# Kernel optimization log

Measured on AMD Instinct MI355X. Metric: run time of the kernel, lower is better.

The kernel has to match this reference:

```python
import jax, jax.numpy as jnp
import numpy as np

# db1 (Haar) filters, replicating the torch module's pywt-derived constants.
_s = np.float32(1.0 / np.sqrt(2.0))
_dl = np.array([_s, _s], np.float32)    # dec_lo[::-1]
_dh = np.array([_s, -_s], np.float32)   # dec_hi[::-1]
_rl = np.array([_s, _s], np.float32)    # rec_lo
_rh = np.array([_s, -_s], np.float32)   # rec_hi
# filters[k][i,j] = a[j]*b[i]  (torch: a.unsqueeze(0)*b.unsqueeze(1)) == outer(b, a)
DEC = jnp.asarray(np.stack([np.outer(_dl, _dl) / 2.0, np.outer(_dh, _dl), np.outer(_dl, _dh), np.outer(_dh, _dh)], 0))  # [4,2,2]
REC = jnp.asarray(np.stack([np.outer(_rl, _rl) * 2.0, np.outer(_rh, _rl), np.outer(_rl, _rh), np.outer(_rh, _rh)], 0))  # [4,2,2]


def wt(x):
    # stride-2 2x2 conv per channel == linear mix of 2x2 blocks; fused over all channels
    B, C, H, W = x.shape
    xb = x.reshape(B, C, H // 2, 2, W // 2, 2)
    y = jnp.einsum('kpq,bchpwq->bckhw', DEC, xb)  # [B,C,4,H/2,W/2]
    y = jnp.concatenate([y[:, :, :1], (y[:, :, 1:] + 1.0) * 0.5], axis=2)  # rescale HF bands
    return y.reshape(B, 4 * C, H // 2, W // 2)


def iwt(y):
    B, C4, H, W = y.shape
    C = C4 // 4
    yb = y.reshape(B, C, 4, H, W)
    yb = jnp.concatenate([yb[:, :, :1], 2.0 * yb[:, :, 1:] - 1.0], axis=2)  # undo HF rescale
    x = jnp.einsum('kpq,bckhw->bchpwq', REC, yb)  # conv_transpose2d, stride 2, no overlap
    return x.reshape(B, C, 2 * H, 2 * W)


def conv3x3(x, w, b):
    y = jax.lax.conv_general_dilated(x, w, (1, 1), ((1, 1), (1, 1)), dimension_numbers=('NCHW', 'OIHW', 'NCHW'))
    return y + b[None, :, None, None]


def setup_inputs() -> dict:
    key = jax.random.key(0)
    ks = jax.random.split(key, 20)
    B, Cin, H, W = 8, 1, 512, 512
    c = 16
    inp = {'x': jax.random.normal(ks[0], (B, Cin, H, W), jnp.float32)}
    specs = [('conv1', c, 4 * Cin), ('conv2', 4 * c, 4 * c), ('conv3', 16 * c, 16 * c), ('conv4', 64 * c, 64 * c),
             ('convd1', 4, c), ('convd2', c, 2 * c), ('convd3', 4 * c, 8 * c), ('convd4', 16 * c, 32 * c)]
    for idx, (name, o, i) in enumerate(specs):
        kw, kb = jax.random.split(ks[1 + idx])
        inp[name + '_w'] = jax.random.normal(kw, (o, i, 3, 3), jnp.float32) / np.float32(np.sqrt(i * 9))
        inp[name + '_b'] = jax.random.normal(kb, (o,), jnp.float32) * 0.01
    return inp


def reference(x, conv1_w, conv1_b, conv2_w, conv2_b, conv3_w, conv3_b, conv4_w, conv4_b,
              convd1_w, convd1_b, convd2_w, convd2_b, convd3_w, convd3_b, convd4_w, convd4_b):
    lrelu = lambda t: jax.nn.leaky_relu(t, 0.2)
    w1 = wt(x);  c1 = lrelu(conv3x3(w1, conv1_w, conv1_b))
    w2 = wt(c1); c2 = lrelu(conv3x3(w2, conv2_w, conv2_b))
    w3 = wt(c2); c3 = lrelu(conv3x3(w3, conv3_w, conv3_b))
    w4 = wt(c3); c4 = lrelu(conv3x3(w4, conv4_w, conv4_b))
    c5 = lrelu(conv3x3(c4, conv4_w, conv4_b))  # conv4 reused, as in the torch module
    c6 = conv3x3(c5, conv4_w, conv4_b)
    ic4 = lrelu(c6 + w4)
    ic3 = lrelu(conv3x3(jnp.concatenate([c3, iwt(ic4)], 1), convd4_w, convd4_b))
    ic2 = lrelu(conv3x3(jnp.concatenate([c2, iwt(ic3)], 1), convd3_w, convd3_b))
    ic1 = lrelu(conv3x3(jnp.concatenate([c1, iwt(ic2)], 1), convd2_w, convd2_b))
    iw1 = lrelu(conv3x3(ic1, convd1_w, convd1_b))
    logits = iwt(iw1)
    return jax.nn.sigmoid(logits)
```

## Files before the change

kernel.cpp:

```cpp
#include <hip/hip_runtime.h>
#include <cstddef>


typedef unsigned short u16;
typedef unsigned int u32;
typedef __bf16 bf16x8 __attribute__((ext_vector_type(8)));
typedef float floatx4 __attribute__((ext_vector_type(4)));
typedef u16 u16x4 __attribute__((ext_vector_type(4)));
typedef u16 u16x8 __attribute__((ext_vector_type(8)));

__device__ __forceinline__ float b2f(u16 h) {
    union { u32 u; float f; } x; x.u = ((u32)h) << 16; return x.f;
}
__device__ __forceinline__ u16 f2b(float f) {
    union { float f; u32 u; } x; x.f = f;
    return (u16)((x.u + 0x7FFFu + ((x.u >> 16) & 1u)) >> 16);
}
__device__ __forceinline__ float lrelu_f(float v) { return v > 0.f ? v : 0.2f * v; }

__device__ __forceinline__ void gld16(const u16* g, u16* l) {
    __builtin_amdgcn_global_load_lds(
        (const __attribute__((address_space(1))) u32*)(const void*)g,
        (__attribute__((address_space(3))) u32*)(void*)l, 16, 0, 0);
}

__global__ __launch_bounds__(512, 4)
void conv_mfma8_k(const u16* __restrict__ in, int Cin, int iWp, int iImg,
                  const u16* __restrict__ wb, const float* __restrict__ bias,
                  const u16* __restrict__ skip, int sC, int sWp, int sImg, int spad,
                  u16* __restrict__ out, int Cst, int oWp, int oImg, int opad,
                  int logW, int logH)
{
    __shared__ alignas(16) u16 S[32768];

    const int tid = threadIdx.x;
    const int wid = tid >> 6, lane = tid & 63;
    const int half = wid >> 2, wl = wid & 3;
    const int W = 1 << logW, H = 1 << logH;
    const int mBase = blockIdx.x * 128;
    const int nBase = blockIdx.y * 128;
    const int K = 9 * Cin;
    const int nChunks = K / 32;
    const int nC = nChunks >> 1;

    const int kg = lane & 3;
    const int rr = lane >> 2;
    const int kgs = kg ^ ((rr >> 1) & 3);

    const int k0 = half * nC * 32;
    int tap = k0 / Cin;
    int cbn = k0 - tap * Cin;

    const u16 *gA0, *gA1, *gB0, *gB1;
    {
        int ty = tap / 3, tx = tap - ty * 3;
        int m0 = mBase + wl * 32 + rr;
        int px0 = m0 & (W - 1), py0 = (m0 >> logW) & (H - 1), pb0 = m0 >> (logW + logH);
        gA0 = in + ((size_t)pb0 * iImg + (size_t)(py0 + ty) * iWp + (px0 + tx)) * Cin + cbn + kgs * 8;
        int m1 = m0 + 16;
        int px1 = m1 & (W - 1), py1 = (m1 >> logW) & (H - 1), pb1 = m1 >> (logW + logH);
        gA1 = in + ((size_t)pb1 * iImg + (size_t)(py1 + ty) * iWp + (px1 + tx)) * Cin + cbn + kgs * 8;
    }
    gB0 = wb + (size_t)(nBase + wl * 32 + rr) * K + k0 + kgs * 8;
    gB1 = wb + (size_t)(nBase + wl * 32 + 16 + rr) * K + k0 + kgs * 8;

    u16* Sb = &S[half * 16384];
    u16* lA0 = Sb + wl * 1024;
    u16* lA1 = Sb + wl * 1024 + 512;
    u16* lB0 = Sb + 8192 + wl * 1024;
    u16* lB1 = Sb + 8192 + wl * 1024 + 512;

    const int wm = wl >> 1, wn = wl & 1;
    const int fm = lane & 15;
    const int fk = ((lane >> 4) * 8) ^ (((fm >> 1) & 3) << 3);

    floatx4 acc[4][4] = {};

    const size_t rowStep = (size_t)(iWp - 2) * Cin;

    auto stage = [&](int buf) {
        gld16(gA0, lA0 + buf * 4096);
        gld16(gA1, lA1 + buf * 4096);
        gld16(gB0, lB0 + buf * 4096);
        gld16(gB1, lB1 + buf * 4096);
        size_t dA = 32;
        cbn += 32;
        if (cbn == Cin) { cbn = 0; ++tap; dA = ((tap % 3 == 0) ? rowStep : (size_t)Cin) - (size_t)(Cin - 32); }
        gA0 += dA; gA1 += dA;
        gB0 += 32; gB1 += 32;
    };

    auto compute = [&](int buf) {
        const u16* Ab = Sb + buf * 4096;
        const u16* Bb = Sb + 8192 + buf * 4096;
        bf16x8 af[4], bfr[4];
#pragma unroll
        for (int mt = 0; mt < 4; ++mt)
            af[mt] = *(const bf16x8*)&Ab[(wm * 64 + mt * 16 + fm) * 32 + fk];
#pragma unroll
        for (int nt = 0; nt < 4; ++nt)
            bfr[nt] = *(const bf16x8*)&Bb[(wn * 64 + nt * 16 + fm) * 32 + fk];
        __builtin_amdgcn_s_setprio(1);
#pragma unroll
        for (int mt = 0; mt < 4; ++mt)
#pragma unroll
            for (int nt = 0; nt < 4; ++nt)
                acc[mt][nt] = __builtin_amdgcn_mfma_f32_16x16x32_bf16(af[mt], bfr[nt], acc[mt][nt], 0, 0, 0);
        __builtin_amdgcn_s_setprio(0);
    };

    stage(0);
    __syncthreads();
    for (int kc = 0; kc < nC; kc += 2) {
        stage(1);
        compute(0);
        __syncthreads();
        if (kc + 2 < nC) stage(0);
        compute(1);
        __syncthreads();
    }

    float* R = (float*)S;
    if (half == 1) {
#pragma unroll
        for (int mt = 0; mt < 4; ++mt)
#pragma unroll
            for (int nt = 0; nt < 4; ++nt) {
                int j = mt * 4 + nt;
                *(floatx4*)&R[(size_t)(((wl * 16 + j) * 64) + lane) * 4] = acc[mt][nt];
            }
    }
    __syncthreads();
    if (half == 0) {
        const int rq = (lane >> 4) * 4;
#pragma unroll
        for (int mt = 0; mt < 4; ++mt)
#pragma unroll
            for (int nt = 0; nt < 4; ++nt) {
                int j = mt * 4 + nt;
                floatx4 v = *(const floatx4*)&R[(size_t)(((wl * 16 + j) * 64) + lane) * 4];
                acc[mt][nt] = acc[mt][nt] + v;
            }
#pragma unroll
        for (int mt = 0; mt < 4; ++mt) {
            const int mrow = mBase + wm * 64 + mt * 16 + rq;
#pragma unroll
            for (int r = 0; r < 4; ++r) {
                int m2 = mrow + r;
                int px = m2 & (W - 1), py = (m2 >> logW) & (H - 1), pb2 = m2 >> (logW + logH);
                size_t ob = ((size_t)pb2 * oImg + (size_t)(py + opad) * oWp + (px + opad)) * Cst;
                size_t sb = 0;
                if (skip) sb = ((size_t)pb2 * sImg + (size_t)(py + spad) * sWp + (px + spad)) * sC;
#pragma unroll
                for (int nt = 0; nt < 4; ++nt) {
                    int n = nBase + wn * 64 + nt * 16 + fm;
                    float v = acc[mt][nt][r] + bias[n];
                    if (skip) v += b2f(skip[sb + n]);
                    v = lrelu_f(v);
                    out[ob + n] = f2b(v);
                }
            }
        }
    }
}

__global__ __launch_bounds__(256)
void conv_mfma_k(const u16* __restrict__ in, int Cin, int iWp, int iImg,
                 const u16* __restrict__ wb, const float* __restrict__ bias,
                 const u16* __restrict__ skip, int sC, int sWp, int sImg, int spad,
                 u16* __restrict__ out, int Cst, int oWp, int oImg, int opad,
                 int logW, int logH)
{
    constexpr int NT = 2;
    constexpr int BM = 128, BN = NT * 32;
    constexpr int ASZ = BM * 32;
    constexpr int BSZ = BN * 32;
    __shared__ u16 At[2 * ASZ];
    __shared__ u16 Bt[2 * BSZ];

    const int tid = threadIdx.x;
    const int wid = tid >> 6, lane = tid & 63;
    const int W = 1 << logW, H = 1 << logH;
    const int mBase = blockIdx.x * BM;
    const int nBase = blockIdx.y * BN;
    const int K = 9 * Cin;
    const int kg = lane & 3;
    const int rr = lane >> 2;
    const int kgs = kg ^ ((rr >> 1) & 3);

    const u16 *gA0, *gA1, *gB0;
    {
        int m0 = mBase + wid * 32 + rr;
        int px0 = m0 & (W - 1), py0 = (m0 >> logW) & (H - 1), pb0 = m0 >> (logW + logH);
        gA0 = in + ((size_t)pb0 * iImg + (size_t)py0 * iWp + px0) * Cin + kgs * 8;
        int m1 = m0 + 16;
        int px1 = m1 & (W - 1), py1 = (m1 >> logW) & (H - 1), pb1 = m1 >> (logW + logH);
        gA1 = in + ((size_t)pb1 * iImg + (size_t)py1 * iWp + px1) * Cin + kgs * 8;
    }
    gB0 = wb + (size_t)(nBase + wid * 16 + rr) * K + kgs * 8;
    u16* lA0 = &At[wid * 1024];
    u16* lA1 = &At[wid * 1024 + 512];
    u16* lB0 = &Bt[wid * 512];

    const int wm = wid >> 1, wn = wid & 1;
    const int fm = lane & 15;
    const int fk = ((lane >> 4) * 8) ^ (((fm >> 1) & 3) << 3);

    floatx4 acc[4][NT] = {};

    const int nChunks = K / 32;
    const size_t rowStep = (size_t)(iWp - 2) * Cin;
    int cbn = 0, tap = 0;

    auto stage = [&](int buf) {
        gld16(gA0, lA0 + buf * ASZ);
        gld16(gA1, lA1 + buf * ASZ);
        gld16(gB0, lB0 + buf * BSZ);
        size_t dA = 32;
        cbn += 32;
        if (cbn == Cin) { cbn = 0; ++tap; dA = ((tap % 3 == 0) ? rowStep : (size_t)Cin) - (size_t)(Cin - 32); }
        gA0 += dA; gA1 += dA;
        gB0 += 32;
    };

    auto compute = [&](int buf) {
        const u16* Ab = &At[buf * ASZ];
        const u16* Bb = &Bt[buf * BSZ];
        bf16x8 af[4], bfr[NT];
#pragma unroll
        for (int mt = 0; mt < 4; ++mt)
            af[mt] = *(const bf16x8*)&Ab[(wm * 64 + mt * 16 + fm) * 32 + fk];
#pragma unroll
        for (int nt = 0; nt < NT; ++nt)
            bfr[nt] = *(const bf16x8*)&Bb[(wn * (NT * 16) + nt * 16 + fm) * 32 + fk];
        __builtin_amdgcn_s_setprio(1);
#pragma unroll
        for (int mt = 0; mt < 4; ++mt)
#pragma unroll
            for (int nt = 0; nt < NT; ++nt)
                acc[mt][nt] = __builtin_amdgcn_mfma_f32_16x16x32_bf16(af[mt], bfr[nt], acc[mt][nt], 0, 0, 0);
        __builtin_amdgcn_s_setprio(0);
    };

    stage(0);
    __syncthreads();
    for (int kc = 0; kc < nChunks; kc += 2) {
        stage(1);
        compute(0);
        __syncthreads();
        if (kc + 2 < nChunks) stage(0);
        compute(1);
        __syncthreads();
    }

    const int rq = (lane >> 4) * 4;
#pragma unroll
    for (int mt = 0; mt < 4; ++mt) {
        const int mrow = mBase + wm * 64 + mt * 16 + rq;
#pragma unroll
        for (int r = 0; r < 4; ++r) {
            int m2 = mrow + r;
            int px = m2 & (W - 1), py = (m2 >> logW) & (H - 1), pb2 = m2 >> (logW + logH);
            size_t ob = ((size_t)pb2 * oImg + (size_t)(py + opad) * oWp + (px + opad)) * Cst;
            size_t sb = 0;
            if (skip) sb = ((size_t)pb2 * sImg + (size_t)(py + spad) * sWp + (px + spad)) * sC;
#pragma unroll
            for (int nt = 0; nt < NT; ++nt) {
                int n = nBase + wn * (NT * 16) + nt * 16 + fm;
                float v = acc[mt][nt][r] + bias[n];
                if (skip) v += b2f(skip[sb + n]);
                v = lrelu_f(v);
                out[ob + n] = f2b(v);
            }
        }
    }
}

__global__ __launch_bounds__(256)
void conv_n16_k(const u16* __restrict__ in, int iWp, int iImg,
                const u16* __restrict__ wb, const float* __restrict__ bias,
                u16* __restrict__ out, int logW, int logH)
{
    __shared__ u16 At[128 * 32];
    __shared__ u16 Bt[16 * 32];
    const int tid = threadIdx.x;
    const int wid = tid >> 6, lane = tid & 63;
    const int W = 1 << logW, H = 1 << logH;
    const int mBase = blockIdx.x * 128;
    const int kg = lane & 3, rr = lane >> 2;
    const int kgs = kg ^ ((rr >> 1) & 3);

    const u16 *gA0, *gA1;
    {
        int m0 = mBase + wid * 32 + rr;
        int px0 = m0 & (W - 1), py0 = (m0 >> logW) & (H - 1), pb0 = m0 >> (logW + logH);
        gA0 = in + ((size_t)pb0 * iImg + (size_t)py0 * iWp + px0) * 32 + kgs * 8;
        int m1 = m0 + 16;
        int px1 = m1 & (W - 1), py1 = (m1 >> logW) & (H - 1), pb1 = m1 >> (logW + logH);
        gA1 = in + ((size_t)pb1 * iImg + (size_t)py1 * iWp + px1) * 32 + kgs * 8;
    }
    const u16* gB = wb + (size_t)rr * 288 + kgs * 8;
    u16* lA0 = &At[wid * 1024];
    u16* lA1 = &At[wid * 1024 + 512];

    const int fm = lane & 15;
    const int fk = ((lane >> 4) * 8) ^ (((fm >> 1) & 3) << 3);
    floatx4 acc[2] = {};
    const size_t rowStep = (size_t)(iWp - 2) * 32;

    for (int tap = 0; tap < 9; ++tap) {
        gld16(gA0, lA0);
        gld16(gA1, lA1);
        if (wid == 0) gld16(gB, &Bt[0]);
        __syncthreads();
        bf16x8 bf = *(const bf16x8*)&Bt[fm * 32 + fk];
#pragma unroll
        for (int mt = 0; mt < 2; ++mt) {
            bf16x8 af = *(const bf16x8*)&At[(wid * 32 + mt * 16 + fm) * 32 + fk];
            acc[mt] = __builtin_amdgcn_mfma_f32_16x16x32_bf16(af, bf, acc[mt], 0, 0, 0);
        }
        __syncthreads();
        size_t dA = (tap % 3 == 2) ? rowStep : (size_t)32;
        gA0 += dA; gA1 += dA; gB += 32;
    }

    const int rq = (lane >> 4) * 4;
    const float bn = bias[fm];
#pragma unroll
    for (int mt = 0; mt < 2; ++mt) {
#pragma unroll
        for (int r = 0; r < 4; ++r) {
            int m2 = mBase + wid * 32 + mt * 16 + rq + r;
            out[(size_t)m2 * 16 + fm] = f2b(lrelu_f(acc[mt][r] + bn));
        }
    }
}

template<int CIN, int COUT>
__global__ __launch_bounds__(256)
void conv_direct_k(const u16* __restrict__ in, int Sin,
                   const float* __restrict__ w, const float* __restrict__ bias,
                   u16* __restrict__ out, int Sout, int oWp, int oImg, int opad,
                   int logW, int logH, int total)
{
    int m = blockIdx.x * 256 + threadIdx.x;
    if (m >= total) return;
    const int W = 1 << logW, H = 1 << logH;
    const int px = m & (W - 1);
    const int py = (m >> logW) & (H - 1);
    const int pb = m >> (logW + logH);
    float acc[COUT];
#pragma unroll
    for (int o = 0; o < COUT; ++o) acc[o] = bias[o];
    for (int tap = 0; tap < 9; ++tap) {
        int dy = tap / 3 - 1, dx = tap % 3 - 1;
        int iy = py + dy, ix = px + dx;
        if ((unsigned)iy >= (unsigned)H || (unsigned)ix >= (unsigned)W) continue;
        const u16* p = in + (size_t)((((pb << logH) + iy) << logW) + ix) * Sin;
        if constexpr (CIN == 4) {
            u16x4 v = *(const u16x4*)p;
#pragma unroll
            for (int ci = 0; ci < 4; ++ci) {
                float f = b2f(v[ci]);
#pragma unroll
                for (int o = 0; o < COUT; ++o) acc[o] += f * w[(o * CIN + ci) * 9 + tap];
            }
        } else {
#pragma unroll
            for (int c8 = 0; c8 < CIN / 8; ++c8) {
                u16x8 v = *(const u16x8*)(p + c8 * 8);
#pragma unroll
                for (int j = 0; j < 8; ++j) {
                    int ci = c8 * 8 + j;
                    float f = b2f(v[j]);
#pragma unroll
                    for (int o = 0; o < COUT; ++o) acc[o] += f * w[(o * CIN + ci) * 9 + tap];
                }
            }
        }
    }
    size_t ob = ((size_t)pb * oImg + (size_t)(py + opad) * oWp + (px + opad)) * Sout;
#pragma unroll
    for (int o = 0; o < COUT; ++o)
        out[ob + o] = f2b(lrelu_f(acc[o]));
}

__global__ __launch_bounds__(256)
void wt_in_k(const float* __restrict__ x, u16* __restrict__ out, int total)
{
    int idx = blockIdx.x * 256 + threadIdx.x;
    if (idx >= total) return;
    int wq = idx & 255, t = idx >> 8;
    int hq = t & 255, b = t >> 8;
    const float* p = x + ((size_t)b * 512 + 2 * hq) * 512 + 2 * wq;
    float a = p[0], bv = p[1], cv = p[512], d = p[513];
    u16x4 o = { f2b(0.25f * (a + bv + cv + d)),
                f2b(0.25f * (a + bv - cv - d) + 0.5f),
                f2b(0.25f * (a - bv + cv - d) + 0.5f),
                f2b(0.25f * (a - bv - cv + d) + 0.5f) };
    *(u16x4*)&out[(size_t)idx * 4] = o;
}

__global__ __launch_bounds__(256)
void wt_k(const u16* __restrict__ in, int Sin, int iWp, int iImg, int ipad,
          u16* __restrict__ out, int Sout, int oWp, int oImg, int opad,
          int logC, int logWo, int logHo, int total)
{
    int idx = blockIdx.x * 256 + threadIdx.x;
    if (idx >= total) return;
    const int C = 1 << logC, Wo = 1 << logWo, Ho = 1 << logHo;
    int c = idx & (C - 1); int t = idx >> logC;
    int wq = t & (Wo - 1); t >>= logWo;
    int hq = t & (Ho - 1); int b = t >> logHo;
    size_t p00 = ((size_t)b * iImg + (size_t)(2 * hq + ipad) * iWp + (2 * wq + ipad)) * Sin + c;
    float a  = b2f(in[p00]);
    float bv = b2f(in[p00 + Sin]);
    float cv = b2f(in[p00 + (size_t)iWp * Sin]);
    float d  = b2f(in[p00 + (size_t)iWp * Sin + Sin]);
    u16x4 o = { f2b(0.25f * (a + bv + cv + d)),
                f2b(0.25f * (a + bv - cv - d) + 0.5f),
                f2b(0.25f * (a - bv + cv - d) + 0.5f),
                f2b(0.25f * (a - bv - cv + d) + 0.5f) };
    *(u16x4*)&out[((size_t)b * oImg + (size_t)(hq + opad) * oWp + (wq + opad)) * Sout + 4 * c] = o;
}

__global__ __launch_bounds__(256)
void iwt_k(const u16* __restrict__ in, int Sin, int logC, int logW, int logH,
           u16* __restrict__ out, int Sout, int oWp, int oImg, int opad, int total)
{
    int idx = blockIdx.x * 256 + threadIdx.x;
    if (idx >= total) return;
    const int C = 1 << logC, W = 1 << logW;
    int c = idx & (C - 1); int t = idx >> logC;
    int wq = t & (W - 1); t >>= logW;
    int hq = t & ((1 << logH) - 1); int b = t >> logH;
    u16x4 v = *(const u16x4*)&in[(size_t)((((b << logH) + hq) << logW) + wq) * Sin + 4 * c];
    float y0 = b2f(v[0]);
    float y1 = 2.f * b2f(v[1]) - 1.f;
    float y2 = 2.f * b2f(v[2]) - 1.f;
    float y3 = 2.f * b2f(v[3]) - 1.f;
    float x00 = y0 + 0.5f * ( y1 + y2 + y3);
    float x01 = y0 + 0.5f * ( y1 - y2 - y3);
    float x10 = y0 + 0.5f * (-y1 + y2 - y3);
    float x11 = y0 + 0.5f * (-y1 - y2 + y3);
    size_t q = ((size_t)b * oImg + (size_t)(2 * hq + opad) * oWp + (2 * wq + opad)) * Sout + c;
    out[q] = f2b(x00);
    out[q + Sout] = f2b(x01);
    out[q + (size_t)oWp * Sout] = f2b(x10);
    out[q + (size_t)oWp * Sout + Sout] = f2b(x11);
}

__global__ __launch_bounds__(256)
void iwt_out_k(const u16* __restrict__ in, float* __restrict__ out, int total)
{
    int idx = blockIdx.x * 256 + threadIdx.x;
    if (idx >= total) return;
    int wq = idx & 255, t = idx >> 8;
    int hq = t & 255, b = t >> 8;
    u16x4 v = *(const u16x4*)&in[(size_t)idx * 4];
    float y0 = b2f(v[0]);
    float y1 = 2.f * b2f(v[1]) - 1.f;
    float y2 = 2.f * b2f(v[2]) - 1.f;
    float y3 = 2.f * b2f(v[3]) - 1.f;
    float x00 = y0 + 0.5f * ( y1 + y2 + y3);
    float x01 = y0 + 0.5f * ( y1 - y2 - y3);
    float x10 = y0 + 0.5f * (-y1 + y2 - y3);
    float x11 = y0 + 0.5f * (-y1 - y2 + y3);
    float* q = out + ((size_t)b * 512 + 2 * hq) * 512 + 2 * wq;
    q[0]   = 1.f / (1.f + __expf(-x00));
    q[1]   = 1.f / (1.f + __expf(-x01));
    q[512] = 1.f / (1.f + __expf(-x10));
    q[513] = 1.f / (1.f + __expf(-x11));
}

__global__ __launch_bounds__(256)
void prep_w_k(const float* __restrict__ src, u16* __restrict__ dst, int logCIN, int total)
{
    int idx = blockIdx.x * 256 + threadIdx.x;
    if (idx >= total) return;
    const int CIN = 1 << logCIN;
    int ci = idx & (CIN - 1);
    int q = idx >> logCIN;
    int tap = q % 9, o = q / 9;
    dst[idx] = f2b(src[((size_t)(o * CIN + ci)) * 9 + tap]);
}

__global__ __launch_bounds__(256)
void zb_k(u16* __restrict__ buf, int Wp, int Hp, int C, int total)
{
    int idx = blockIdx.x * 256 + threadIdx.x;
    if (idx >= total) return;
    int c8 = idx % (C / 8); int t = idx / (C / 8);
    int nbp = 2 * Wp + 2 * (Hp - 2);
    int p = t % nbp; int b = t / nbp;
    int y, x;
    if (p < Wp) { y = 0; x = p; }
    else if (p < 2 * Wp) { y = Hp - 1; x = p - Wp; }
    else { int q = p - 2 * Wp; y = 1 + (q >> 1); x = (q & 1) ? Wp - 1 : 0; }
    u16x8 z = {0, 0, 0, 0, 0, 0, 0, 0};
    *(u16x8*)&buf[((size_t)b * Hp * Wp + (size_t)y * Wp + x) * C + c8 * 8] = z;
}

extern "C" void kernel_launch(void* const* d_in, const int* in_sizes, int n_in,
                              void* d_out, int out_size, void* d_ws, size_t ws_size,
                              hipStream_t stream)
{
    const float* x   = (const float*)d_in[0];
    const float* c1w = (const float*)d_in[1];  const float* c1b = (const float*)d_in[2];
    const float* c2w = (const float*)d_in[3];  const float* c2b = (const float*)d_in[4];
    const float* c3w = (const float*)d_in[5];  const float* c3b = (const float*)d_in[6];
    const float* c4w = (const float*)d_in[7];  const float* c4b = (const float*)d_in[8];
    const float* d1w = (const float*)d_in[9];  const float* d1b = (const float*)d_in[10];
    const float* d2w = (const float*)d_in[11]; const float* d2b = (const float*)d_in[12];
    const float* d3w = (const float*)d_in[13]; const float* d3b = (const float*)d_in[14];
    const float* d4w = (const float*)d_in[15]; const float* d4b = (const float*)d_in[16];

    const size_t MiB = 1u << 20;
    char* base = (char*)d_ws;
    u16* c4wb = (u16*)base;
    u16* c3wb = c4wb + 9437184;
    u16* d4wb = c3wb + 589824;
    u16* d3wb = d4wb + 1179648;
    u16* c2wb = d3wb + 73728;
    u16* d2wb = c2wb + 36864;
    u16* CAT1p = (u16*)(base + 22  * MiB);
    u16* CAT2p = (u16*)(base + 55  * MiB);
    u16* CAT3p = (u16*)(base + 88  * MiB);
    u16* P1    = (u16*)(base + 123 * MiB);
    u16* P2    = (u16*)(base + 142 * MiB);
    u16* P3    = (u16*)(base + 161 * MiB);
    float* outp = (float*)d_out;

    u16* W2p = P1; u16* W4p = P1; u16* IC2 = P1;
    u16* W3p = P2; u16* C4p = P2; u16* IC4 = P2; u16* IC1 = P2;
    u16* W1  = P3; u16* C5p = P3; u16* IC3 = P3; u16* IW1 = P3;

    auto cdiv = [](int a, int b) { return (a + b - 1) / b; };
    auto prep = [&](const float* s, u16* d, int logCIN, int total) {
        prep_w_k<<<cdiv(total, 256), 256, 0, stream>>>(s, d, logCIN, total);
    };
    auto zb = [&](u16* buf, int Wp, int Hp, int C) {
        int total = 8 * (2 * Wp + 2 * (Hp - 2)) * (C / 8);
        zb_k<<<cdiv(total, 256), 256, 0, stream>>>(buf, Wp, Hp, C, total);
    };
    auto mfma = [&](const u16* in, int Cin, int iWp, int iImg,
                    const u16* w, const float* bi,
                    const u16* skip, int sC, int sWp, int sImg, int spad,
                    int Cout, u16* out, int Cst, int oWp, int oImg, int opad,
                    int logW, int logH) {
        int M = 8 << (logW + logH);
        if (Cout % 128 == 0) {
            dim3 g(M / 128, Cout / 128);
            conv_mfma8_k<<<g, 512, 0, stream>>>(in, Cin, iWp, iImg, w, bi,
                                                skip, sC, sWp, sImg, spad,
                                                out, Cst, oWp, oImg, opad, logW, logH);
        } else {
            dim3 g(M / 128, Cout / 64);
            conv_mfma_k<<<g, 256, 0, stream>>>(in, Cin, iWp, iImg, w, bi,
                                               skip, sC, sWp, sImg, spad,
                                               out, Cst, oWp, oImg, opad, logW, logH);
        }
    };

    prep(c4w, c4wb, 10, 9437184);
    prep(c3w, c3wb, 8, 589824);
    prep(d4w, d4wb, 9, 1179648);
    prep(d3w, d3wb, 7, 73728);
    prep(c2w, c2wb, 6, 36864);
    prep(d2w, d2wb, 5, 4608);
    zb(CAT1p, 258, 258, 32);
    zb(W2p, 130, 130, 64);
    zb(W3p, 66, 66, 256);
    zb(CAT2p, 130, 130, 128);
    zb(CAT3p, 66, 66, 512);

    const int P256 = 8 * 256 * 256;
    const int T2M = 2097152;
    const int I258 = 258 * 258;

    wt_in_k<<<cdiv(P256, 256), 256, 0, stream>>>(x, W1, P256);
    conv_direct_k<4, 16><<<cdiv(P256, 256), 256, 0, stream>>>(
        W1, 4, c1w, c1b, CAT1p, 32, 258, I258, 1, 8, 8, P256);
    zb(C5p, 34, 34, 1024);
    wt_k<<<cdiv(T2M, 256), 256, 0, stream>>>(CAT1p, 32, 258, I258, 1,
                                             W2p, 64, 130, 16900, 1, 4, 7, 7, T2M);
    mfma(W2p, 64, 130, 16900, c2wb, c2b, nullptr, 0, 0, 0, 0,
         64, CAT2p, 128, 130, 16900, 1, 7, 7);
    zb(W4p, 34, 34, 1024);
    wt_k<<<cdiv(T2M, 256), 256, 0, stream>>>(CAT2p, 128, 130, 16900, 1,
                                             W3p, 256, 66, 4356, 1, 6, 6, 6, T2M);
    mfma(W3p, 256, 66, 4356, c3wb, c3b, nullptr, 0, 0, 0, 0,
         256, CAT3p, 512, 66, 4356, 1, 6, 6);
    zb(C4p, 34, 34, 1024);
    wt_k<<<cdiv(T2M, 256), 256, 0, stream>>>(CAT3p, 512, 66, 4356, 1,
                                             W4p, 1024, 34, 1156, 1, 8, 5, 5, T2M);
    mfma(W4p, 1024, 34, 1156, c4wb, c4b, nullptr, 0, 0, 0, 0,
         1024, C4p, 1024, 34, 1156, 1, 5, 5);
    mfma(C4p, 1024, 34, 1156, c4wb, c4b, nullptr, 0, 0, 0, 0,
         1024, C5p, 1024, 34, 1156, 1, 5, 5);
    mfma(C5p, 1024, 34, 1156, c4wb, c4b, W4p, 1024, 34, 1156, 1,
         1024, IC4, 1024, 32, 1024, 0, 5, 5);
    iwt_k<<<cdiv(T2M, 256), 256, 0, stream>>>(IC4, 1024, 8, 5, 5,
                                              CAT3p + 256, 512, 66, 4356, 1, T2M);
    mfma(CAT3p, 512, 66, 4356, d4wb, d4b, nullptr, 0, 0, 0, 0,
         256, IC3, 256, 64, 4096, 0, 6, 6);
    iwt_k<<<cdiv(T2M, 256), 256, 0, stream>>>(IC3, 256, 6, 6, 6,
                                              CAT2p + 64, 128, 130, 16900, 1, T2M);
    mfma(CAT2p, 128, 130, 16900, d3wb, d3b, nullptr, 0, 0, 0, 0,
         64, IC2, 64, 128, 16384, 0, 7, 7);
    iwt_k<<<cdiv(T2M, 256), 256, 0, stream>>>(IC2, 64, 4, 7, 7,
                                              CAT1p + 16, 32, 258, I258, 1, T2M);
    conv_n16_k<<<dim3(P256 / 128), 256, 0, stream>>>(CAT1p, 258, I258, d2wb, d2b, IC1, 8, 8);
    conv_direct_k<16, 4><<<cdiv(P256, 256), 256, 0, stream>>>(
        IC1, 16, d1w, d1b, IW1, 4, 256, 65536, 0, 8, 8, P256);
    iwt_out_k<<<cdiv(P256, 256), 256, 0, stream>>>(IW1, outp, P256);
}
```

Baseline: 1.009 ms.

## Replace split-K 128x128 conv tile with 256x128 tile and deeper LDS pipeline

Rewrites the wide-channel implicit-GEMM conv kernel. The old kernel split K across two 4-wave halves and reduced partial sums through LDS. The new one has all 8 waves cover a 256x128 output tile over the full K, with 4 A buffers and 6 B buffers in a rotating multi-stage pipeline. It replaces __syncthreads with raw s_waitcnt vmcnt(2)+s_barrier so loads can stay in flight, which removes the cross-half reduction and reuses each B tile across more rows. The cost is much larger LDS use, lower occupancy (launch bounds 2), and an unrolled schedule that assumes K/32 is a multiple of 12 and at least 12.

Result: slower. 1.079 ms (+7.0%).

```diff
diff --git a/kernel.cpp b/kernel.cpp
--- a/kernel.cpp
+++ b/kernel.cpp
@@ -24,75 +24,73 @@
         (__attribute__((address_space(3))) u32*)(void*)l, 16, 0, 0);
 }
 
-__global__ __launch_bounds__(512, 4)
-void conv_mfma8_k(const u16* __restrict__ in, int Cin, int iWp, int iImg,
-                  const u16* __restrict__ wb, const float* __restrict__ bias,
-                  const u16* __restrict__ skip, int sC, int sWp, int sImg, int spad,
-                  u16* __restrict__ out, int Cst, int oWp, int oImg, int opad,
-                  int logW, int logH)
-{
-    __shared__ alignas(16) u16 S[32768];
+#define WB2 asm volatile("s_waitcnt vmcnt(2) lgkmcnt(0)\ns_barrier" ::: "memory")
+#define WB0 asm volatile("s_waitcnt vmcnt(0) lgkmcnt(0)\ns_barrier" ::: "memory")
+
+__global__ __launch_bounds__(512, 2)
+void conv_mfma8w_k(const u16* __restrict__ in, int Cin, int iWp, int iImg,
+                   const u16* __restrict__ wb, const float* __restrict__ bias,
+                   const u16* __restrict__ skip, int sC, int sWp, int sImg, int spad,
+                   u16* __restrict__ out, int Cst, int oWp, int oImg, int opad,
+                   int logW, int logH)
+{
+    constexpr int ASZ = 256 * 32;
+    constexpr int BSZ = 128 * 32;
+    __shared__ u16 At[4 * ASZ];
+    __shared__ u16 Bt[6 * BSZ];
 
     const int tid = threadIdx.x;
     const int wid = tid >> 6, lane = tid & 63;
-    const int half = wid >> 2, wl = wid & 3;
     const int W = 1 << logW, H = 1 << logH;
-    const int mBase = blockIdx.x * 128;
+    const int mBase = blockIdx.x * 256;
     const int nBase = blockIdx.y * 128;
     const int K = 9 * Cin;
-    const int nChunks = K / 32;
-    const int nC = nChunks >> 1;
-
     const int kg = lane & 3;
     const int rr = lane >> 2;
     const int kgs = kg ^ ((rr >> 1) & 3);
 
-    const int k0 = half * nC * 32;
-    int tap = k0 / Cin;
-    int cbn = k0 - tap * Cin;
-
-    const u16 *gA0, *gA1, *gB0, *gB1;
+    const u16 *gA0, *gA1, *gB0;
     {
-        int ty = tap / 3, tx = tap - ty * 3;
-        int m0 = mBase + wl * 32 + rr;
+        int m0 = mBase + wid * 32 + rr;
         int px0 = m0 & (W - 1), py0 = (m0 >> logW) & (H - 1), pb0 = m0 >> (logW + logH);
-        gA0 = in + ((size_t)pb0 * iImg + (size_t)(py0 + ty) * iWp + (px0 + tx)) * Cin + cbn + kgs * 8;
+        gA0 = in + ((size_t)pb0 * iImg + (size_t)py0 * iWp + px0) * Cin + kgs * 8;
         int m1 = m0 + 16;
         int px1 = m1 & (W - 1), py1 = (m1 >> logW) & (H - 1), pb1 = m1 >> (logW + logH);
-        gA1 = in + ((size_t)pb1 * iImg + (size_t)(py1 + ty) * iWp + (px1 + tx)) * Cin + cbn + kgs * 8;
-    }
-    gB0 = wb + (size_t)(nBase + wl * 32 + rr) * K + k0 + kgs * 8;
-    gB1 = wb + (size_t)(nBase + wl * 32 + 16 + rr) * K + k0 + kgs * 8;
-
-    u16* Sb = &S[half * 16384];
-    u16* lA0 = Sb + wl * 1024;
-    u16* lA1 = Sb + wl * 1024 + 512;
-    u16* lB0 = Sb + 8192 + wl * 1024;
-    u16* lB1 = Sb + 8192 + wl * 1024 + 512;
-
-    const int wm = wl >> 1, wn = wl & 1;
+        gA1 = in + ((size_t)pb1 * iImg + (size_t)py1 * iWp + px1) * Cin + kgs * 8;
+    }
+    gB0 = wb + (size_t)(nBase + wid * 16 + rr) * K + kgs * 8;
+
+    u16* lA0 = &At[wid * 1024];
+    u16* lA1 = &At[wid * 1024 + 512];
+    u16* lB0 = &Bt[wid * 512];
+
+    const int wm = wid >> 1, wn = wid & 1;
     const int fm = lane & 15;
     const int fk = ((lane >> 4) * 8) ^ (((fm >> 1) & 3) << 3);
 
     floatx4 acc[4][4] = {};
 
+    const int nChunks = K / 32;
     const size_t rowStep = (size_t)(iWp - 2) * Cin;
-
-    auto stage = [&](int buf) {
-        gld16(gA0, lA0 + buf * 4096);
-        gld16(gA1, lA1 + buf * 4096);
-        gld16(gB0, lB0 + buf * 4096);
-        gld16(gB1, lB1 + buf * 4096);
+    int cbn = 0, tap = 0;
+
+    auto stageA = [&](int buf) {
+        gld16(gA0, lA0 + buf * ASZ);
+        gld16(gA1, lA1 + buf * ASZ);
         size_t dA = 32;
         cbn += 32;
         if (cbn == Cin) { cbn = 0; ++tap; dA = ((tap % 3 == 0) ? rowStep : (size_t)Cin) - (size_t)(Cin - 32); }
         gA0 += dA; gA1 += dA;
-        gB0 += 32; gB1 += 32;
-    };
-
-    auto compute = [&](int buf) {
-        const u16* Ab = Sb + buf * 4096;
-        const u16* Bb = Sb + 8192 + buf * 4096;
+    };
+
+    auto stageB = [&](int buf) {
+        gld16(gB0, lB0 + buf * BSZ);
+        gB0 += 32;
+    };
+
+    auto compute = [&](int ab, int bb) {
+        const u16* Ab = &At[ab * ASZ];
+        const u16* Bb = &Bt[bb * BSZ];
         bf16x8 af[4], bfr[4];
 #pragma unroll
         for (int mt = 0; mt < 4; ++mt)
@@ -109,56 +107,43 @@
         __builtin_amdgcn_s_setprio(0);
     };
 
-    stage(0);
-    __syncthreads();
-    for (int kc = 0; kc < nC; kc += 2) {
-        stage(1);
-        compute(0);
-        __syncthreads();
-        if (kc + 2 < nC) stage(0);
-        compute(1);
-        __syncthreads();
-    }
-
-    float* R = (float*)S;
-    if (half == 1) {
-#pragma unroll
-        for (int mt = 0; mt < 4; ++mt)
+    stageA(0); stageA(1);
+    stageB(0); stageB(1); stageB(2); stageB(3);
+    WB2;
+    const int nMac = nChunks / 12;
+    for (int it = 0; it < nMac - 1; ++it) {
+        stageA(2); stageA(3); stageB(4); stageB(5); compute(0, 0); compute(1, 1); WB2;
+        stageA(0); stageA(1); stageB(0); stageB(1); compute(2, 2); compute(3, 3); WB2;
+        stageA(2); stageA(3); stageB(2); stageB(3); compute(0, 4); compute(1, 5); WB2;
+        stageA(0); stageA(1); stageB(4); stageB(5); compute(2, 0); compute(3, 1); WB2;
+        stageA(2); stageA(3); stageB(0); stageB(1); compute(0, 2); compute(1, 3); WB2;
+        stageA(0); stageA(1); stageB(2); stageB(3); compute(2, 4); compute(3, 5); WB2;
+    }
+    stageA(2); stageA(3); stageB(4); stageB(5); compute(0, 0); compute(1, 1); WB2;
+    stageA(0); stageA(1); stageB(0); stageB(1); compute(2, 2); compute(3, 3); WB2;
+    stageA(2); stageA(3); stageB(2); stageB(3); compute(0, 4); compute(1, 5); WB2;
+    stageA(0); stageA(1); stageB(4); stageB(5); compute(2, 0); compute(3, 1); WB2;
+    stageA(2); stageA(3);                       compute(0, 2); compute(1, 3); WB0;
+    compute(2, 4); compute(3, 5);
+
+    const int rq = (lane >> 4) * 4;
+#pragma unroll
+    for (int mt = 0; mt < 4; ++mt) {
+        const int mrow = mBase + wm * 64 + mt * 16 + rq;
+#pragma unroll
+        for (int r = 0; r < 4; ++r) {
+            int m2 = mrow + r;
+            int px = m2 & (W - 1), py = (m2 >> logW) & (H - 1), pb2 = m2 >> (logW + logH);
+            size_t ob = ((size_t)pb2 * oImg + (size_t)(py + opad) * oWp + (px + opad)) * Cst;
+            size_t sb = 0;
+            if (skip) sb = ((size_t)pb2 * sImg + (size_t)(py + spad) * sWp + (px + spad)) * sC;
 #pragma unroll
             for (int nt = 0; nt < 4; ++nt) {
-                int j = mt * 4 + nt;
-                *(floatx4*)&R[(size_t)(((wl * 16 + j) * 64) + lane) * 4] = acc[mt][nt];
-            }
-    }
-    __syncthreads();
-    if (half == 0) {
-        const int rq = (lane >> 4) * 4;
-#pragma unroll
-        for (int mt = 0; mt < 4; ++mt)
-#pragma unroll
-            for (int nt = 0; nt < 4; ++nt) {
-                int j = mt * 4 + nt;
-                floatx4 v = *(const floatx4*)&R[(size_t)(((wl * 16 + j) * 64) + lane) * 4];
-                acc[mt][nt] = acc[mt][nt] + v;
-            }
-#pragma unroll
-        for (int mt = 0; mt < 4; ++mt) {
-            const int mrow = mBase + wm * 64 + mt * 16 + rq;
-#pragma unroll
-            for (int r = 0; r < 4; ++r) {
-                int m2 = mrow + r;
-                int px = m2 & (W - 1), py = (m2 >> logW) & (H - 1), pb2 = m2 >> (logW + logH);
-                size_t ob = ((size_t)pb2 * oImg + (size_t)(py + opad) * oWp + (px + opad)) * Cst;
-                size_t sb = 0;
-                if (skip) sb = ((size_t)pb2 * sImg + (size_t)(py + spad) * sWp + (px + spad)) * sC;
-#pragma unroll
-                for (int nt = 0; nt < 4; ++nt) {
-                    int n = nBase + wn * 64 + nt * 16 + fm;
-                    float v = acc[mt][nt][r] + bias[n];
-                    if (skip) v += b2f(skip[sb + n]);
-                    v = lrelu_f(v);
-                    out[ob + n] = f2b(v);
-                }
+                int n = nBase + wn * 64 + nt * 16 + fm;
+                float v = acc[mt][nt][r] + bias[n];
+                if (skip) v += b2f(skip[sb + n]);
+                v = lrelu_f(v);
+                out[ob + n] = f2b(v);
             }
         }
     }
@@ -550,10 +535,10 @@
                     int logW, int logH) {
         int M = 8 << (logW + logH);
         if (Cout % 128 == 0) {
-            dim3 g(M / 128, Cout / 128);
-            conv_mfma8_k<<<g, 512, 0, stream>>>(in, Cin, iWp, iImg, w, bi,
-                                                skip, sC, sWp, sImg, spad,
-                                                out, Cst, oWp, oImg, opad, logW, logH);
+            dim3 g(M / 256, Cout / 128);
+            conv_mfma8w_k<<<g, 512, 0, stream>>>(in, Cin, iWp, iImg, w, bi,
+                                                 skip, sC, sWp, sImg, spad,
+                                                 out, Cst, oWp, oImg, opad, logW, logH);
         } else {
             dim3 g(M / 128, Cout / 64);
             conv_mfma_k<<<g, 256, 0, stream>>>(in, Cin, iWp, iImg, w, bi,
```
